# Performance work log

Hardware: AMD Instinct MI355X
Metric: run time of the kernel (lower is better)

The kernel has to match this reference:

```python
import jax, jax.numpy as jnp
import numpy as np

N_NODES = 15135


def setup_inputs() -> dict:
    key = jax.random.key(0)
    ks = jax.random.split(key, 12)
    bs, N, F_in, H, L, Hfc, C, E = 8, N_NODES, 64, 128, 3, 512, 10, 242160
    s = lambda k, *sh: jax.random.normal(k, sh, dtype=jnp.float32) * 0.05
    return {
        "x": jax.random.normal(ks[0], (bs, N, F_in), dtype=jnp.float32),
        "edge_index": jax.random.randint(ks[1], (2, E), 0, N),
        "W1": s(ks[2], F_in, H), "b1": jnp.zeros((H,), jnp.float32),
        "W2": s(ks[3], H, H),   "b2": jnp.zeros((H,), jnp.float32),
        "W3": s(ks[4], H, H),   "b3": jnp.zeros((H,), jnp.float32),
        "Wfc": s(ks[5], L * H, 1), "bfc": jnp.zeros((1,), jnp.float32),
        "Wl1": s(ks[6], N, Hfc), "bl1": jnp.zeros((Hfc,), jnp.float32),
        "Wl2": s(ks[7], Hfc, C), "bl2": jnp.zeros((C,), jnp.float32),
    }


def _gcn_norm(edge_index, num_nodes):
    # add self loops, compute symmetric normalization (PyG GCNConv default)
    loop = jnp.arange(num_nodes, dtype=edge_index.dtype)
    src = jnp.concatenate([edge_index[0], loop])
    dst = jnp.concatenate([edge_index[1], loop])
    deg = jax.ops.segment_sum(jnp.ones_like(dst, dtype=jnp.float32), dst,
                              num_segments=num_nodes)
    dinv = jax.lax.rsqrt(deg)  # deg >= 1 due to self-loops
    norm = dinv[src] * dinv[dst]
    return src, dst, norm


def _gcn_conv(x, W, b, src, dst, norm):
    # x: [bs, N, Fin] -> [bs, N, Fout]
    xl = jnp.einsum("bnf,fh->bnh", x, W)
    msg = xl[:, src, :] * norm[None, :, None]  # [bs, E+N, Fout]
    out = jnp.zeros_like(xl).at[:, dst].add(msg)
    return out + b


def reference(x, edge_index, W1, b1, W2, b2, W3, b3, Wfc, bfc, Wl1, bl1, Wl2, bl2):
    bs, N, _ = x.shape
    src, dst, norm = _gcn_norm(edge_index, N)
    h1 = jax.nn.relu(_gcn_conv(x, W1, b1, src, dst, norm))
    h2 = jax.nn.relu(_gcn_conv(h1, W2, b2, src, dst, norm))
    h3 = jax.nn.relu(_gcn_conv(h2, W3, b3, src, dst, norm))
    # mode='cat': torch.stack(xs, -1).view(bs, N, -1) interleaves features
    hcat = jnp.stack([h1, h2, h3], axis=-1).reshape(bs, N, -1)  # [bs,N,H*L]
    g = (jnp.einsum("bnk,ko->bno", hcat, Wfc) + bfc).reshape(bs, N)
    # dropout layers are identity in eval mode
    z = jax.nn.relu(g @ Wl1 + bl1)
    logits = z @ Wl2 + bl2
    return jax.nn.log_softmax(logits, axis=-1)
```

## Files before the change

kernel.cpp:

```cpp
#include <hip/hip_runtime.h>
#include <hip/hip_bf16.h>

#define NN 15135
#define BS 8
#define FIN 64
#define HD 128
#define EE 242160
#define HFC 512
#define NCLS 10

#define M_ROWS (BS * NN)
#define M_PAD  121088
#define PADE   287616

typedef __attribute__((ext_vector_type(8))) short bf16x8;
typedef __attribute__((ext_vector_type(4))) float f32x4;

__device__ __forceinline__ unsigned short to_bf16(float f) {
    unsigned u = __float_as_uint(f);
    u = (u + 0x7fffu + ((u >> 16) & 1u)) >> 16;
    return (unsigned short)u;
}
__device__ __forceinline__ unsigned pack2_bf16(float lo, float hi) {
    unsigned a = __float_as_uint(lo);
    unsigned b = __float_as_uint(hi);
    a = (a + 0x7fffu + ((a >> 16) & 1u)) >> 16;
    b = (b + 0x7fffu + ((b >> 16) & 1u)) & 0xffff0000u;
    return (a & 0xffffu) | b;
}

__global__ void k_deg(const int* __restrict__ dst, int* __restrict__ degi) {
    int e = blockIdx.x * 256 + threadIdx.x;
    if (e < EE) atomicAdd(&degi[dst[e]], 1);
}

#define SCAN_T 1024
#define SCAN_PER 15
__global__ __launch_bounds__(SCAN_T) void k_scan(const int* __restrict__ degi,
                                                 int* __restrict__ row_ptr,
                                                 float* __restrict__ dinv) {
    __shared__ int part[SCAN_T];
    const int t = threadIdx.x;
    const int base = t * SCAN_PER;
    int loc[SCAN_PER];
    int s = 0;
#pragma unroll
    for (int i = 0; i < SCAN_PER; i++) {
        int d = (base + i < NN) ? degi[base + i] : 0;
        if (base + i < NN) dinv[base + i] = rsqrtf((float)d + 1.0f);
        int pd = (d + 3) & ~3;
        loc[i] = s; s += pd;
    }
    part[t] = s;
    __syncthreads();
    for (int off = 1; off < SCAN_T; off <<= 1) {
        int v = (t >= off) ? part[t - off] : 0;
        __syncthreads();
        part[t] += v;
        __syncthreads();
    }
    int before = (t == 0) ? 0 : part[t - 1];
#pragma unroll
    for (int i = 0; i < SCAN_PER; i++)
        if (base + i < NN) row_ptr[base + i] = before + loc[i];
    if (t == SCAN_T - 1) row_ptr[NN] = part[SCAN_T - 1];
}

__global__ void k_bucket(const int* __restrict__ src, const int* __restrict__ dst,
                         const int* __restrict__ row_ptr, int* __restrict__ cursor,
                         const float* __restrict__ dinv,
                         int* __restrict__ s_idx, float* __restrict__ wts) {
    int e = blockIdx.x * 256 + threadIdx.x;
    if (e >= EE) return;
    int s = src[e], d = dst[e];
    int pos = atomicAdd(&cursor[d], 1);
    int idx = row_ptr[d] + pos;
    s_idx[idx] = s;
    wts[idx] = dinv[s] * dinv[d];
}

__global__ void k_cvtX(const float* __restrict__ x, unsigned* __restrict__ xb) {
    int g = blockIdx.x * 256 + threadIdx.x;
    float2 v = *(const float2*)&x[(size_t)g * 2];
    xb[g] = pack2_bf16(v.x, v.y);
}

__global__ void k_cvtW(const float* __restrict__ W1, const float* __restrict__ W2,
                       const float* __restrict__ W3, unsigned short* __restrict__ Wt) {
    int idx = blockIdx.x * 256 + threadIdx.x;
    const float* W; int K, base;
    if (idx < 8192)       { W = W1; K = 64;  base = idx; }
    else if (idx < 24576) { W = W2; K = 128; base = idx - 8192; }
    else                  { W = W3; K = 128; base = idx - 24576; }
    int c = base / K, k = base % K;
    Wt[idx] = to_bf16(W[(size_t)k * HD + c]);
}

template<int F>
__global__ __launch_bounds__(256) void k_agg(const unsigned short* __restrict__ Xb,
                                             const int* __restrict__ row_ptr,
                                             const int* __restrict__ s_idx,
                                             const float* __restrict__ wts,
                                             const float* __restrict__ dinv,
                                             unsigned short* __restrict__ Ab) {
    constexpr int LPB = F / 2;
    constexpr int BPW = 64 / LPB;
    const int tid = threadIdx.x;
    const int widx = tid >> 6, lane = tid & 63;
    const int n = blockIdx.x * 4 + widx;
    if (n >= NN) return;
    const int bb = blockIdx.y * BPW + lane / LPB;
    const int fp = lane % LPB;
    const unsigned short* Xs = Xb + (size_t)bb * NN * F + 2 * fp;

    const int e0 = __builtin_amdgcn_readfirstlane(row_ptr[n]);
    const int e1 = __builtin_amdgcn_readfirstlane(row_ptr[n + 1]);
    const float dv = dinv[n];

    float ax, ay;
    {
        unsigned u = *(const unsigned*)&Xs[(size_t)n * F];
        float w0 = dv * dv;
        ax = w0 * __uint_as_float(u << 16);
        ay = w0 * __uint_as_float(u & 0xffff0000u);
    }
    for (int c = e0; c < e1; c += 4) {
        int s0 = s_idx[c + 0], s1 = s_idx[c + 1], s2 = s_idx[c + 2], s3 = s_idx[c + 3];
        float w0 = wts[c + 0], w1 = wts[c + 1], w2 = wts[c + 2], w3 = wts[c + 3];
        unsigned u0 = *(const unsigned*)&Xs[(size_t)s0 * F];
        unsigned u1 = *(const unsigned*)&Xs[(size_t)s1 * F];
        unsigned u2 = *(const unsigned*)&Xs[(size_t)s2 * F];
        unsigned u3 = *(const unsigned*)&Xs[(size_t)s3 * F];
        ax += w0 * __uint_as_float(u0 << 16); ay += w0 * __uint_as_float(u0 & 0xffff0000u);
        ax += w1 * __uint_as_float(u1 << 16); ay += w1 * __uint_as_float(u1 & 0xffff0000u);
        ax += w2 * __uint_as_float(u2 << 16); ay += w2 * __uint_as_float(u2 & 0xffff0000u);
        ax += w3 * __uint_as_float(u3 << 16); ay += w3 * __uint_as_float(u3 & 0xffff0000u);
    }
    *(unsigned*)&Ab[(size_t)bb * NN * F + (size_t)n * F + 2 * fp] = pack2_bf16(ax, ay);
}

template<int KD, int LIDX, bool GINIT, bool STOREH>
__global__ __launch_bounds__(256) void k_gemm_ep(const unsigned short* __restrict__ Xb,
                                                 const unsigned short* __restrict__ Wt,
                                                 const float* __restrict__ bias,
                                                 const float* __restrict__ Wfc,
                                                 const float* __restrict__ bfc,
                                                 unsigned short* __restrict__ H,
                                                 float* __restrict__ g) {
    constexpr int NK = KD / 32;
    const int tid = threadIdx.x;
    const int w = tid >> 6, lane = tid & 63;
    const int l15 = lane & 15, lhi = lane >> 4;
    const int row0 = blockIdx.x * 64;
    const int cbase = w * 32;

    bf16x8 B[2][NK];
#pragma unroll
    for (int ct = 0; ct < 2; ct++)
#pragma unroll
        for (int ks = 0; ks < NK; ks++)
            B[ct][ks] = *(const bf16x8*)&Wt[(size_t)(cbase + ct * 16 + l15) * KD + ks * 32 + lhi * 8];

    f32x4 acc[4][2] = {};
#pragma unroll
    for (int ks = 0; ks < NK; ks++) {
        bf16x8 A[4];
#pragma unroll
        for (int rt = 0; rt < 4; rt++)
            A[rt] = *(const bf16x8*)&Xb[(size_t)(row0 + rt * 16 + l15) * KD + ks * 32 + lhi * 8];
#pragma unroll
        for (int rt = 0; rt < 4; rt++)
#pragma unroll
            for (int ct = 0; ct < 2; ct++)
                acc[rt][ct] = __builtin_amdgcn_mfma_f32_16x16x32_bf16(A[rt], B[ct][ks], acc[rt][ct], 0, 0, 0);
    }

    __shared__ float gred[4][64];
    const float bias0 = bias[cbase + l15], bias1 = bias[cbase + 16 + l15];
    const float wf0 = Wfc[(cbase + l15) * 3 + LIDX];
    const float wf1 = Wfc[(cbase + 16 + l15) * 3 + LIDX];
#pragma unroll
    for (int rt = 0; rt < 4; rt++) {
#pragma unroll
        for (int reg = 0; reg < 4; reg++) {
            const int row = row0 + rt * 16 + lhi * 4 + reg;
            float h0 = fmaxf(acc[rt][0][reg] + bias0, 0.f);
            float h1 = fmaxf(acc[rt][1][reg] + bias1, 0.f);
            if (STOREH) {
                H[(size_t)row * 128 + cbase + l15] = to_bf16(h0);
                H[(size_t)row * 128 + cbase + 16 + l15] = to_bf16(h1);
            }
            float p = h0 * wf0 + h1 * wf1;
#pragma unroll
            for (int m = 8; m; m >>= 1) p += __shfl_xor(p, m, 64);
            if (l15 == 0) gred[w][rt * 16 + lhi * 4 + reg] = p;
        }
    }
    __syncthreads();
    if (tid < 64) {
        const int row = row0 + tid;
        if (row < M_ROWS) {
            float s = gred[0][tid] + gred[1][tid] + gred[2][tid] + gred[3][tid];
            if (GINIT) g[row] = bfc[0] + s; else g[row] += s;
        }
    }
}

#define FC1_CH 473
__global__ __launch_bounds__(256) void k_fc1part(const float* __restrict__ g,
                                                 const float* __restrict__ Wl1,
                                                 float* __restrict__ part) {
    const int c = blockIdx.x * 64 + (threadIdx.x & 63);
    const int nq = threadIdx.x >> 6;
    const int n0 = blockIdx.y * FC1_CH;
    const int n1 = min(n0 + FC1_CH, NN);
    float acc[BS];
#pragma unroll
    for (int b = 0; b < BS; b++) acc[b] = 0.f;
    for (int n = n0 + nq; n < n1; n += 4) {
        float w = Wl1[(size_t)n * HFC + c];
#pragma unroll
        for (int b = 0; b < BS; b++) acc[b] += g[b * NN + n] * w;
    }
    __shared__ float red[4][64][BS];
    const int cl = threadIdx.x & 63;
#pragma unroll
    for (int b = 0; b < BS; b++) red[nq][cl][b] = acc[b];
    __syncthreads();
    if (nq == 0) {
#pragma unroll
        for (int b = 0; b < BS; b++) {
            float s = red[0][cl][b] + red[1][cl][b] + red[2][cl][b] + red[3][cl][b];
            part[((size_t)blockIdx.y * HFC + c) * BS + b] = s;
        }
    }
}

__global__ __launch_bounds__(512) void k_fc1red_head(const float* __restrict__ part,
                                                     const float* __restrict__ bl1,
                                                     const float* __restrict__ Wl2,
                                                     const float* __restrict__ bl2,
                                                     float* __restrict__ out) {
    __shared__ float zs[HFC * BS];
    __shared__ float lg[BS * NCLS];
    const int c = threadIdx.x;
    float acc[BS];
#pragma unroll
    for (int b = 0; b < BS; b++) acc[b] = 0.f;
    for (int y = 0; y < 32; y++) {
#pragma unroll
        for (int b = 0; b < BS; b++) acc[b] += part[((size_t)y * HFC + c) * BS + b];
    }
    float bb = bl1[c];
#pragma unroll
    for (int b = 0; b < BS; b++) zs[c * BS + b] = fmaxf(acc[b] + bb, 0.f);
    __syncthreads();
    const int t = threadIdx.x;
    if (t < BS * NCLS) {
        int b = t / NCLS, cc = t % NCLS;
        float a = bl2[cc];
        for (int k = 0; k < HFC; k++) a += zs[k * BS + b] * Wl2[k * NCLS + cc];
        lg[b * NCLS + cc] = a;
    }
    __syncthreads();
    if (t < BS * NCLS) {
        int b = t / NCLS, cc = t % NCLS;
        float m = -1e30f;
#pragma unroll
        for (int j = 0; j < NCLS; j++) m = fmaxf(m, lg[b * NCLS + j]);
        float s = 0.f;
#pragma unroll
        for (int j = 0; j < NCLS; j++) s += expf(lg[b * NCLS + j] - m);
        out[b * NCLS + cc] = lg[b * NCLS + cc] - m - logf(s);
    }
}

extern "C" void kernel_launch(void* const* d_in, const int* in_sizes, int n_in,
                              void* d_out, int out_size, void* d_ws, size_t ws_size,
                              hipStream_t stream) {
    const float* x   = (const float*)d_in[0];
    const int*   ei  = (const int*)d_in[1];
    const float* W1  = (const float*)d_in[2];
    const float* b1  = (const float*)d_in[3];
    const float* W2  = (const float*)d_in[4];
    const float* b2  = (const float*)d_in[5];
    const float* W3  = (const float*)d_in[6];
    const float* b3  = (const float*)d_in[7];
    const float* Wfc = (const float*)d_in[8];
    const float* bfc = (const float*)d_in[9];
    const float* Wl1 = (const float*)d_in[10];
    const float* bl1 = (const float*)d_in[11];
    const float* Wl2 = (const float*)d_in[12];
    const float* bl2 = (const float*)d_in[13];
    float* out = (float*)d_out;

    const int* srcp = ei;
    const int* dstp = ei + EE;

    float* ws = (float*)d_ws;
    float* dinv    = ws;
    float* g       = ws + 15360;
    float* part    = ws + 136448;
    int*   degi    = (int*)(ws + 267520);
    int*   cursor  = (int*)(ws + 282880);
    int*   row_ptr = (int*)(ws + 298240);
    int*   s_idx   = (int*)(ws + 313728);
    float* wts     = ws + 601344;
    unsigned short* Wt  = (unsigned short*)(ws + 888960);
    unsigned short* Wt1 = Wt;
    unsigned short* Wt2 = Wt + 8192;
    unsigned short* Wt3 = Wt + 24576;
    unsigned short* xb  = (unsigned short*)(ws + 909440);
    unsigned short* a0  = (unsigned short*)(ws + 4784256);
    unsigned short* B1  = (unsigned short*)(ws + 8659072);
    unsigned short* B2  = (unsigned short*)(ws + 16408704);

    const int gemm_grid = M_PAD / 64;

    hipMemsetAsync(degi, 0, 2 * 15360 * sizeof(int), stream);
    hipMemsetAsync(s_idx, 0, 2 * PADE * sizeof(int), stream);
    k_deg<<<(EE + 255) / 256, 256, 0, stream>>>(dstp, degi);
    k_scan<<<1, SCAN_T, 0, stream>>>(degi, row_ptr, dinv);
    k_bucket<<<(EE + 255) / 256, 256, 0, stream>>>(srcp, dstp, row_ptr, cursor, dinv, s_idx, wts);

    k_cvtX<<<M_ROWS * FIN / 2 / 256, 256, 0, stream>>>(x, (unsigned*)xb);
    k_cvtW<<<160, 256, 0, stream>>>(W1, W2, W3, Wt);

    k_agg<64><<<dim3((NN + 3) / 4, 4), 256, 0, stream>>>(xb, row_ptr, s_idx, wts, dinv, a0);
    k_gemm_ep<64, 0, true, true><<<gemm_grid, 256, 0, stream>>>(a0, Wt1, b1, Wfc, bfc, B1, g);
    k_agg<128><<<dim3((NN + 3) / 4, 8), 256, 0, stream>>>(B1, row_ptr, s_idx, wts, dinv, B2);
    k_gemm_ep<128, 1, false, true><<<gemm_grid, 256, 0, stream>>>(B2, Wt2, b2, Wfc, bfc, B1, g);
    k_agg<128><<<dim3((NN + 3) / 4, 8), 256, 0, stream>>>(B1, row_ptr, s_idx, wts, dinv, B2);
    k_gemm_ep<128, 2, false, false><<<gemm_grid, 256, 0, stream>>>(B2, Wt3, b3, Wfc, bfc, B1, g);

    k_fc1part<<<dim3(8, 32), 256, 0, stream>>>(g, Wl1, part);
    k_fc1red_head<<<1, 512, 0, stream>>>(part, bl1, Wl2, bl2, out);
}
```

Before: 497.6 us.

## Fuse x bf16 conversion into first aggregation and restructure FC1 reduction

The first aggregation now gathers fp32 input features directly, which removes the separate x-to-bf16 conversion kernel and its intermediate buffer. The FC1 stage is reorganised to use 237 node chunks, with g staged in shared memory, float4 loads of Wl1, and a separate parallel reduction kernel plus a small head kernel. This replaces the single-block reduction over 32 partials. The cost is more gather bytes in the first aggregation (fp32 rather than bf16), a larger partials buffer, and one extra kernel launch.

```diff
diff --git a/kernel.cpp b/kernel.cpp
--- a/kernel.cpp
+++ b/kernel.cpp
@@ -12,6 +12,9 @@
 #define M_ROWS (BS * NN)
 #define M_PAD  121088
 #define PADE   287616
+
+#define NCH 237
+#define NPLANES (NCH * 2)
 
 typedef __attribute__((ext_vector_type(8))) short bf16x8;
 typedef __attribute__((ext_vector_type(4))) float f32x4;
@@ -79,12 +82,6 @@
     wts[idx] = dinv[s] * dinv[d];
 }
 
-__global__ void k_cvtX(const float* __restrict__ x, unsigned* __restrict__ xb) {
-    int g = blockIdx.x * 256 + threadIdx.x;
-    float2 v = *(const float2*)&x[(size_t)g * 2];
-    xb[g] = pack2_bf16(v.x, v.y);
-}
-
 __global__ void k_cvtW(const float* __restrict__ W1, const float* __restrict__ W2,
                        const float* __restrict__ W3, unsigned short* __restrict__ Wt) {
     int idx = blockIdx.x * 256 + threadIdx.x;
@@ -96,30 +93,63 @@
     Wt[idx] = to_bf16(W[(size_t)k * HD + c]);
 }
 
-template<int F>
-__global__ __launch_bounds__(256) void k_agg(const unsigned short* __restrict__ Xb,
-                                             const int* __restrict__ row_ptr,
-                                             const int* __restrict__ s_idx,
-                                             const float* __restrict__ wts,
-                                             const float* __restrict__ dinv,
-                                             unsigned short* __restrict__ Ab) {
-    constexpr int LPB = F / 2;
-    constexpr int BPW = 64 / LPB;
+__global__ __launch_bounds__(256) void k_aggx(const float* __restrict__ x,
+                                              const int* __restrict__ row_ptr,
+                                              const int* __restrict__ s_idx,
+                                              const float* __restrict__ wts,
+                                              const float* __restrict__ dinv,
+                                              unsigned short* __restrict__ Ab) {
     const int tid = threadIdx.x;
     const int widx = tid >> 6, lane = tid & 63;
     const int n = blockIdx.x * 4 + widx;
     if (n >= NN) return;
-    const int bb = blockIdx.y * BPW + lane / LPB;
-    const int fp = lane % LPB;
-    const unsigned short* Xs = Xb + (size_t)bb * NN * F + 2 * fp;
+    const int bb = blockIdx.y * 2 + (lane >> 5);
+    const int fp = lane & 31;
+    const float* Xs = x + (size_t)bb * NN * FIN + 2 * fp;
 
     const int e0 = __builtin_amdgcn_readfirstlane(row_ptr[n]);
     const int e1 = __builtin_amdgcn_readfirstlane(row_ptr[n + 1]);
     const float dv = dinv[n];
 
+    float2 v = *(const float2*)&Xs[(size_t)n * FIN];
+    float ax = dv * dv * v.x, ay = dv * dv * v.y;
+
+    for (int c = e0; c < e1; c += 4) {
+        int s0 = s_idx[c + 0], s1 = s_idx[c + 1], s2 = s_idx[c + 2], s3 = s_idx[c + 3];
+        float w0 = wts[c + 0], w1 = wts[c + 1], w2 = wts[c + 2], w3 = wts[c + 3];
+        float2 u0 = *(const float2*)&Xs[(size_t)s0 * FIN];
+        float2 u1 = *(const float2*)&Xs[(size_t)s1 * FIN];
+        float2 u2 = *(const float2*)&Xs[(size_t)s2 * FIN];
+        float2 u3 = *(const float2*)&Xs[(size_t)s3 * FIN];
+        ax += w0 * u0.x; ay += w0 * u0.y;
+        ax += w1 * u1.x; ay += w1 * u1.y;
+        ax += w2 * u2.x; ay += w2 * u2.y;
+        ax += w3 * u3.x; ay += w3 * u3.y;
+    }
+    *(unsigned*)&Ab[(size_t)bb * NN * FIN + (size_t)n * FIN + 2 * fp] = pack2_bf16(ax, ay);
+}
+
+__global__ __launch_bounds__(256) void k_agg128(const unsigned short* __restrict__ Xb,
+                                                const int* __restrict__ row_ptr,
+                                                const int* __restrict__ s_idx,
+                                                const float* __restrict__ wts,
+                                                const float* __restrict__ dinv,
+                                                unsigned short* __restrict__ Ab) {
+    const int tid = threadIdx.x;
+    const int widx = tid >> 6, lane = tid & 63;
+    const int n = blockIdx.x * 4 + widx;
+    if (n >= NN) return;
+    const int bb = blockIdx.y;
+    const int fp = lane;
+    const unsigned short* Xs = Xb + (size_t)bb * NN * HD + 2 * fp;
+
+    const int e0 = __builtin_amdgcn_readfirstlane(row_ptr[n]);
+    const int e1 = __builtin_amdgcn_readfirstlane(row_ptr[n + 1]);
+    const float dv = dinv[n];
+
     float ax, ay;
     {
-        unsigned u = *(const unsigned*)&Xs[(size_t)n * F];
+        unsigned u = *(const unsigned*)&Xs[(size_t)n * HD];
         float w0 = dv * dv;
         ax = w0 * __uint_as_float(u << 16);
         ay = w0 * __uint_as_float(u & 0xffff0000u);
@@ -127,16 +157,16 @@
     for (int c = e0; c < e1; c += 4) {
         int s0 = s_idx[c + 0], s1 = s_idx[c + 1], s2 = s_idx[c + 2], s3 = s_idx[c + 3];
         float w0 = wts[c + 0], w1 = wts[c + 1], w2 = wts[c + 2], w3 = wts[c + 3];
-        unsigned u0 = *(const unsigned*)&Xs[(size_t)s0 * F];
-        unsigned u1 = *(const unsigned*)&Xs[(size_t)s1 * F];
-        unsigned u2 = *(const unsigned*)&Xs[(size_t)s2 * F];
-        unsigned u3 = *(const unsigned*)&Xs[(size_t)s3 * F];
+        unsigned u0 = *(const unsigned*)&Xs[(size_t)s0 * HD];
+        unsigned u1 = *(const unsigned*)&Xs[(size_t)s1 * HD];
+        unsigned u2 = *(const unsigned*)&Xs[(size_t)s2 * HD];
+        unsigned u3 = *(const unsigned*)&Xs[(size_t)s3 * HD];
         ax += w0 * __uint_as_float(u0 << 16); ay += w0 * __uint_as_float(u0 & 0xffff0000u);
         ax += w1 * __uint_as_float(u1 << 16); ay += w1 * __uint_as_float(u1 & 0xffff0000u);
         ax += w2 * __uint_as_float(u2 << 16); ay += w2 * __uint_as_float(u2 & 0xffff0000u);
         ax += w3 * __uint_as_float(u3 << 16); ay += w3 * __uint_as_float(u3 & 0xffff0000u);
     }
-    *(unsigned*)&Ab[(size_t)bb * NN * F + (size_t)n * F + 2 * fp] = pack2_bf16(ax, ay);
+    *(unsigned*)&Ab[(size_t)bb * NN * HD + (size_t)n * HD + 2 * fp] = pack2_bf16(ax, ay);
 }
 
 template<int KD, int LIDX, bool GINIT, bool STOREH>
@@ -206,72 +236,68 @@
     }
 }
 
-#define FC1_CH 473
 __global__ __launch_bounds__(256) void k_fc1part(const float* __restrict__ g,
                                                  const float* __restrict__ Wl1,
                                                  float* __restrict__ part) {
-    const int c = blockIdx.x * 64 + (threadIdx.x & 63);
-    const int nq = threadIdx.x >> 6;
-    const int n0 = blockIdx.y * FC1_CH;
-    const int n1 = min(n0 + FC1_CH, NN);
-    float acc[BS];
-#pragma unroll
-    for (int b = 0; b < BS; b++) acc[b] = 0.f;
-    for (int n = n0 + nq; n < n1; n += 4) {
-        float w = Wl1[(size_t)n * HFC + c];
-#pragma unroll
-        for (int b = 0; b < BS; b++) acc[b] += g[b * NN + n] * w;
-    }
-    __shared__ float red[4][64][BS];
-    const int cl = threadIdx.x & 63;
-#pragma unroll
-    for (int b = 0; b < BS; b++) red[nq][cl][b] = acc[b];
+    const int ct = threadIdx.x & 127;
+    const int st = threadIdx.x >> 7;
+    const int n0 = blockIdx.x * 64;
+    __shared__ float gs[BS][64];
+    for (int i = threadIdx.x; i < BS * 64; i += 256) {
+        int b = i >> 6, j = i & 63;
+        int n = n0 + j;
+        gs[b][j] = (n < NN) ? g[b * NN + n] : 0.f;
+    }
     __syncthreads();
-    if (nq == 0) {
+
+    f32x4 acc[BS] = {};
+    const int jend = min(64, NN - n0);
+#pragma unroll 4
+    for (int j = st; j < jend; j += 2) {
+        f32x4 wv = *(const f32x4*)&Wl1[(size_t)(n0 + j) * HFC + 4 * ct];
 #pragma unroll
         for (int b = 0; b < BS; b++) {
-            float s = red[0][cl][b] + red[1][cl][b] + red[2][cl][b] + red[3][cl][b];
-            part[((size_t)blockIdx.y * HFC + c) * BS + b] = s;
+            float gv = gs[b][j];
+            acc[b] += gv * wv;
         }
     }
-}
-
-__global__ __launch_bounds__(512) void k_fc1red_head(const float* __restrict__ part,
-                                                     const float* __restrict__ bl1,
-                                                     const float* __restrict__ Wl2,
-                                                     const float* __restrict__ bl2,
-                                                     float* __restrict__ out) {
-    __shared__ float zs[HFC * BS];
-    __shared__ float lg[BS * NCLS];
-    const int c = threadIdx.x;
-    float acc[BS];
-#pragma unroll
-    for (int b = 0; b < BS; b++) acc[b] = 0.f;
-    for (int y = 0; y < 32; y++) {
-#pragma unroll
-        for (int b = 0; b < BS; b++) acc[b] += part[((size_t)y * HFC + c) * BS + b];
-    }
-    float bb = bl1[c];
-#pragma unroll
-    for (int b = 0; b < BS; b++) zs[c * BS + b] = fmaxf(acc[b] + bb, 0.f);
-    __syncthreads();
+    float* p = &part[((size_t)(blockIdx.x * 2 + st)) * (BS * HFC)];
+#pragma unroll
+    for (int b = 0; b < BS; b++)
+        *(f32x4*)&p[b * HFC + 4 * ct] = acc[b];
+}
+
+__global__ __launch_bounds__(128) void k_fc1red(const float* __restrict__ part,
+                                                const float* __restrict__ bl1,
+                                                float* __restrict__ z) {
+    const int idx = blockIdx.x * 128 + threadIdx.x;
+    float s = 0.f;
+#pragma unroll 8
+    for (int y = 0; y < NPLANES; y++) s += part[(size_t)y * (BS * HFC) + idx];
+    const int c = idx & 511;
+    z[idx] = fmaxf(s + bl1[c], 0.f);
+}
+
+__global__ void k_head(const float* __restrict__ z, const float* __restrict__ Wl2,
+                       const float* __restrict__ bl2, float* __restrict__ out) {
+    __shared__ float lg[BS][NCLS];
     const int t = threadIdx.x;
     if (t < BS * NCLS) {
-        int b = t / NCLS, cc = t % NCLS;
-        float a = bl2[cc];
-        for (int k = 0; k < HFC; k++) a += zs[k * BS + b] * Wl2[k * NCLS + cc];
-        lg[b * NCLS + cc] = a;
+        int b = t / NCLS, c = t % NCLS;
+        float a = bl2[c];
+        for (int k = 0; k < HFC; k++) a += z[b * HFC + k] * Wl2[k * NCLS + c];
+        lg[b][c] = a;
     }
     __syncthreads();
     if (t < BS * NCLS) {
-        int b = t / NCLS, cc = t % NCLS;
+        int b = t / NCLS, c = t % NCLS;
         float m = -1e30f;
 #pragma unroll
-        for (int j = 0; j < NCLS; j++) m = fmaxf(m, lg[b * NCLS + j]);
+        for (int j = 0; j < NCLS; j++) m = fmaxf(m, lg[b][j]);
         float s = 0.f;
 #pragma unroll
-        for (int j = 0; j < NCLS; j++) s += expf(lg[b * NCLS + j] - m);
-        out[b * NCLS + cc] = lg[b * NCLS + cc] - m - logf(s);
+        for (int j = 0; j < NCLS; j++) s += expf(lg[b][j] - m);
+        out[b * NCLS + c] = lg[b][c] - m - logf(s);
     }
 }
 
@@ -300,20 +326,20 @@
     float* ws = (float*)d_ws;
     float* dinv    = ws;
     float* g       = ws + 15360;
-    float* part    = ws + 136448;
-    int*   degi    = (int*)(ws + 267520);
-    int*   cursor  = (int*)(ws + 282880);
-    int*   row_ptr = (int*)(ws + 298240);
-    int*   s_idx   = (int*)(ws + 313728);
-    float* wts     = ws + 601344;
-    unsigned short* Wt  = (unsigned short*)(ws + 888960);
+    float* z       = ws + 136448;
+    float* part    = ws + 140544;
+    int*   degi    = (int*)(ws + 2082048);
+    int*   cursor  = (int*)(ws + 2097408);
+    int*   row_ptr = (int*)(ws + 2112768);
+    int*   s_idx   = (int*)(ws + 2128256);
+    float* wts     = ws + 2415872;
+    unsigned short* Wt  = (unsigned short*)(ws + 2703488);
     unsigned short* Wt1 = Wt;
     unsigned short* Wt2 = Wt + 8192;
     unsigned short* Wt3 = Wt + 24576;
-    unsigned short* xb  = (unsigned short*)(ws + 909440);
-    unsigned short* a0  = (unsigned short*)(ws + 4784256);
-    unsigned short* B1  = (unsigned short*)(ws + 8659072);
-    unsigned short* B2  = (unsigned short*)(ws + 16408704);
+    unsigned short* a0  = (unsigned short*)(ws + 2723968);
+    unsigned short* B1  = (unsigned short*)(ws + 6598784);
+    unsigned short* B2  = (unsigned short*)(ws + 14348416);
 
     const int gemm_grid = M_PAD / 64;
 
@@ -322,17 +348,16 @@
     k_deg<<<(EE + 255) / 256, 256, 0, stream>>>(dstp, degi);
     k_scan<<<1, SCAN_T, 0, stream>>>(degi, row_ptr, dinv);
     k_bucket<<<(EE + 255) / 256, 256, 0, stream>>>(srcp, dstp, row_ptr, cursor, dinv, s_idx, wts);
-
-    k_cvtX<<<M_ROWS * FIN / 2 / 256, 256, 0, stream>>>(x, (unsigned*)xb);
     k_cvtW<<<160, 256, 0, stream>>>(W1, W2, W3, Wt);
 
-    k_agg<64><<<dim3((NN + 3) / 4, 4), 256, 0, stream>>>(xb, row_ptr, s_idx, wts, dinv, a0);
+    k_aggx<<<dim3((NN + 3) / 4, 4), 256, 0, stream>>>(x, row_ptr, s_idx, wts, dinv, a0);
     k_gemm_ep<64, 0, true, true><<<gemm_grid, 256, 0, stream>>>(a0, Wt1, b1, Wfc, bfc, B1, g);
-    k_agg<128><<<dim3((NN + 3) / 4, 8), 256, 0, stream>>>(B1, row_ptr, s_idx, wts, dinv, B2);
+    k_agg128<<<dim3((NN + 3) / 4, 8), 256, 0, stream>>>(B1, row_ptr, s_idx, wts, dinv, B2);
     k_gemm_ep<128, 1, false, true><<<gemm_grid, 256, 0, stream>>>(B2, Wt2, b2, Wfc, bfc, B1, g);
-    k_agg<128><<<dim3((NN + 3) / 4, 8), 256, 0, stream>>>(B1, row_ptr, s_idx, wts, dinv, B2);
+    k_agg128<<<dim3((NN + 3) / 4, 8), 256, 0, stream>>>(B1, row_ptr, s_idx, wts, dinv, B2);
     k_gemm_ep<128, 2, false, false><<<gemm_grid, 256, 0, stream>>>(B2, Wt3, b3, Wfc, bfc, B1, g);
 
-    k_fc1part<<<dim3(8, 32), 256, 0, stream>>>(g, Wl1, part);
-    k_fc1red_head<<<1, 512, 0, stream>>>(part, bl1, Wl2, bl2, out);
-}
+    k_fc1part<<<NCH, 256, 0, stream>>>(g, Wl1, part);
+    k_fc1red<<<32, 128, 0, stream>>>(part, bl1, z);
+    k_head<<<1, 128, 0, stream>>>(z, Wl2, bl2, out);
+}
```

New measurement: 491.9 us. Within noise of the previous version (-1.1%).
